# Optimization experiments

Measured on AMD Instinct MI355X. Metric: run time of the kernel, lower is better.

Reference implementation:

```python
import jax, jax.numpy as jnp
import numpy as np

N = 50000
E_RAND = 800000
F_IN = 128
HID = 128
HEADS = 8
LAYERS = 2
DH = HID // HEADS  # 16


def setup_inputs() -> dict:
    key = jax.random.key(0)
    ks = jax.random.split(key, 8)
    x = jax.random.normal(ks[0], (N, F_IN), dtype=jnp.float32)
    # random edges + self loops so every row of the segment-softmax is nonempty
    rnd = jax.random.randint(ks[1], (2, E_RAND), 0, N, dtype=jnp.int32)
    loops = jnp.tile(jnp.arange(N, dtype=jnp.int32), (2, 1))
    edge_idx = jnp.concatenate([rnd, loops], axis=1)  # [2, 850000]
    edge_vals = jnp.ones((edge_idx.shape[1],), dtype=jnp.float32)
    # glorot-style params
    enc_W = jax.random.normal(ks[2], (F_IN, HID), dtype=jnp.float32) * np.sqrt(2.0 / (F_IN + HID))
    enc_b = jnp.zeros((HID,), dtype=jnp.float32)
    W_stack = jax.random.normal(ks[3], (LAYERS, HEADS, HID, DH), dtype=jnp.float32) * np.sqrt(2.0 / (HID + DH))
    a_stack = jax.random.normal(ks[4], (LAYERS, HEADS, 2 * DH), dtype=jnp.float32) * np.sqrt(2.0 / (1 + 2 * DH))
    return {"x": x, "edge_idx": edge_idx, "edge_vals": edge_vals,
            "enc_W": enc_W, "enc_b": enc_b, "W_stack": W_stack, "a_stack": a_stack}


def _gat_layer(xin, row, col, edge_vals, W, a):
    # xin: [N, HID]; W: [H, HID, DH]; a: [H, 2*DH]
    n = xin.shape[0]
    h = jnp.einsum('nd,hdf->hnf', xin, W)            # [H, N, DH]
    a_src, a_dst = a[:, :DH], a[:, DH:]
    alpha_src = jnp.einsum('hnf,hf->hn', h, a_src)   # a . h[row] part
    alpha_dst = jnp.einsum('hnf,hf->hn', h, a_dst)   # a . h[col] part
    logits = edge_vals[None, :] * (alpha_src[:, row] + alpha_dst[:, col])  # [H, E]
    e = jnp.exp(jax.nn.leaky_relu(logits, 0.2))      # unnormalized attention
    rowsum = jax.ops.segment_sum(e.T, row, num_segments=n)               # [N, H]
    msg = e[:, :, None] * h[:, col, :]               # [H, E, DH]
    agg = jax.vmap(lambda m: jax.ops.segment_sum(m, row, num_segments=n))(msg)  # [H, N, DH]
    out = agg / rowsum.T[:, :, None]
    return jnp.transpose(out, (1, 0, 2)).reshape(n, -1)  # concat heads -> [N, HID]


def reference(x, edge_idx, edge_vals, enc_W, enc_b, W_stack, a_stack):
    row, col = edge_idx[0], edge_idx[1]
    xc = x @ enc_W + enc_b  # encoder
    L = W_stack.shape[0]
    for ell in range(L):
        out = _gat_layer(xc, row, col, edge_vals, W_stack[ell], a_stack[ell])
        if ell != L - 1:
            out = jax.nn.elu(out)  # feat_drop is identity in eval mode
        xc = out + xc if ell > 0 else out  # use_residual=True
    # single snapshot: stack over T=1 then permute(1,0,2) -> [N, 1, HID]
    return xc[:, None, :]
```

## Files before the change

### kernel.cpp

```cpp
#include <hip/hip_runtime.h>
#include <hip/hip_bf16.h>


typedef __attribute__((ext_vector_type(8))) short short8;
typedef __attribute__((ext_vector_type(4))) float floatx4;
typedef __attribute__((ext_vector_type(2))) float floatx2;

__device__ __forceinline__ unsigned f2u(float f) { return __float_as_uint(f); }
__device__ __forceinline__ float u2f(unsigned u) { return __uint_as_float(u); }
__device__ __forceinline__ unsigned short f2bf_rne(float x) {
    unsigned u = f2u(x);
    unsigned r = (u + 0x7FFF + ((u >> 16) & 1)) >> 16;
    return (unsigned short)r;
}


__global__ void histpack_kernel(const int* __restrict__ row, int* __restrict__ deg,
                                int* __restrict__ rank, int E, int EB,
                                const float* __restrict__ encW,
                                const float* __restrict__ Wstack,
                                short8* __restrict__ Wh, short8* __restrict__ Wl) {
    int b = blockIdx.x;
    if (b < EB) {
        int e = b * 256 + threadIdx.x;
        if (e < E) rank[e] = atomicAdd(&deg[row[e]], 1);
        return;
    }
    int idx = (b - EB) * 256 + threadIdx.x;
    if (idx >= 3 * 2048) return;
    int mat = idx >> 11;
    int r = idx & 2047;
    int lane = r & 63;
    int tile = r >> 6;
    int ct = tile >> 2, kt = tile & 3;
    int ncol = ct * 16 + (lane & 15);
    int k0 = kt * 32 + ((lane >> 4) * 8);
    short8 hv, lv;
#pragma unroll
    for (int j = 0; j < 8; ++j) {
        int k = k0 + j;
        float w = (mat == 0)
            ? encW[k * 128 + ncol]
            : Wstack[(mat - 1) * 16384 + (ncol >> 4) * 2048 + k * 16 + (ncol & 15)];
        unsigned u = f2u(w);
        hv[j] = (short)(u >> 16);
        float hf = u2f(u & 0xFFFF0000u);
        float l = w - hf;
        lv[j] = (short)(f2u(l) >> 16);
    }
    Wh[idx] = hv;
    Wl[idx] = lv;
}

__global__ void gathercv_kernel(const int* __restrict__ perm, const int* __restrict__ colv,
                                const float* __restrict__ ev, int2* __restrict__ csr_cv,
                                int E) {
    int s = blockIdx.x * 256 + threadIdx.x;
    if (s < E) {
        int e = perm[s];
        csr_cv[s] = make_int2(colv[e], __float_as_int(ev[e]));
    }
}


__device__ __forceinline__ void
gemm_body(int bid, const float* __restrict__ A, const short8* __restrict__ Bh,
          const short8* __restrict__ Bl, const float* __restrict__ bias,
          const float* __restrict__ avec, float* __restrict__ Cf,
          unsigned short* __restrict__ Cbf,
          float* __restrict__ asrc, float* __restrict__ adst, int n, int flags) {
    int wave = threadIdx.x >> 6;
    int lane = threadIdx.x & 63;
    int q = lane >> 4;
    int col = lane & 15;
    int n0w = bid * 64 + wave * 16;

    int arow = min(n0w + col, n - 1);
    const float* Arow = A + (size_t)arow * 128;
    int kb = q * 8;
    short8 Ah[4], Al[4];
#pragma unroll
    for (int kt = 0; kt < 4; ++kt) {
        float4 f0 = *(const float4*)(Arow + kt * 32 + kb);
        float4 f1 = *(const float4*)(Arow + kt * 32 + kb + 4);
        float fv[8] = {f0.x, f0.y, f0.z, f0.w, f1.x, f1.y, f1.z, f1.w};
#pragma unroll
        for (int j = 0; j < 8; ++j) {
            unsigned u = f2u(fv[j]);
            Ah[kt][j] = (short)(u >> 16);
            float hf = u2f(u & 0xFFFF0000u);
            float l = fv[j] - hf;
            Al[kt][j] = (short)(f2u(l) >> 16);
        }
    }

    int nbase = n0w + q * 4;
#pragma unroll
    for (int ct = 0; ct < 8; ++ct) {
        short8 bh[4], bl[4];
#pragma unroll
        for (int kt = 0; kt < 4; ++kt) {
            bh[kt] = Bh[(ct * 4 + kt) * 64 + lane];
            bl[kt] = Bl[(ct * 4 + kt) * 64 + lane];
        }
        float bv = (flags & 1) ? bias[ct * 16 + col] : 0.f;
        floatx4 acc = {bv, bv, bv, bv};
#pragma unroll
        for (int kt = 0; kt < 4; ++kt) {
            acc = __builtin_amdgcn_mfma_f32_16x16x32_bf16(Ah[kt], bh[kt], acc, 0, 0, 0);
            acc = __builtin_amdgcn_mfma_f32_16x16x32_bf16(Al[kt], bh[kt], acc, 0, 0, 0);
            acc = __builtin_amdgcn_mfma_f32_16x16x32_bf16(Ah[kt], bl[kt], acc, 0, 0, 0);
        }
#pragma unroll
        for (int reg = 0; reg < 4; ++reg) {
            int node = nbase + reg;
            if (node < n) {
                if (flags & 4) Cbf[(size_t)node * 128 + ct * 16 + col] = f2bf_rne(acc[reg]);
                else           Cf[(size_t)node * 128 + ct * 16 + col] = acc[reg];
            }
        }
        if (flags & 2) {
            float a_s = avec[ct * 32 + col];
            float a_d = avec[ct * 32 + 16 + col];
#pragma unroll
            for (int reg = 0; reg < 4; ++reg) {
                float ps = acc[reg] * a_s;
                float pd = acc[reg] * a_d;
#pragma unroll
                for (int off = 8; off; off >>= 1) {
                    ps += __shfl_down(ps, off, 16);
                    pd += __shfl_down(pd, off, 16);
                }
                int node = nbase + reg;
                if (col == 0 && node < n) {
                    asrc[node * 8 + ct] = ps;
                    adst[node * 8 + ct] = pd;
                }
            }
        }
    }
}

__global__ __launch_bounds__(256) void
gemm_mfma(const float* __restrict__ A, const short8* __restrict__ Bh,
          const short8* __restrict__ Bl, const float* __restrict__ avec,
          unsigned short* __restrict__ Cbf,
          float* __restrict__ asrc, float* __restrict__ adst, int n) {
    gemm_body(blockIdx.x, A, Bh, Bl, nullptr, avec, nullptr, Cbf, asrc, adst, n, 2 | 4);
}

__global__ __launch_bounds__(256) void
enc_scan_kernel(const float* __restrict__ x, const short8* __restrict__ Wh,
                const short8* __restrict__ Wl, const float* __restrict__ encb,
                float* __restrict__ xc, int n, int GBn,
                const int* __restrict__ deg, int* __restrict__ rowptr) {
    if ((int)blockIdx.x < GBn) {
        gemm_body(blockIdx.x, x, Wh, Wl, encb, nullptr, xc, nullptr,
                  nullptr, nullptr, n, 1);
        return;
    }
    __shared__ int sd[256];
    __shared__ int sbase;
    int t = threadIdx.x;
    int cb = blockIdx.x - GBn;
    int lim = cb * 256;
    const int4* deg4 = (const int4*)deg;
    int lim4 = lim >> 2;
    int b0 = 0, b1 = 0, b2 = 0, b3 = 0;
    for (int k = t; k < lim4; k += 256) {
        int4 d = deg4[k];
        b0 += d.x; b1 += d.y; b2 += d.z; b3 += d.w;
    }
    sd[t] = (b0 + b1) + (b2 + b3);
    __syncthreads();
    for (int off = 128; off; off >>= 1) {
        if (t < off) sd[t] += sd[t + off];
        __syncthreads();
    }
    if (t == 0) sbase = sd[0];
    __syncthreads();
    int idx = lim + t;
    int v = (idx < n) ? deg[idx] : 0;
    sd[t] = v;
    __syncthreads();
    for (int off = 1; off < 256; off <<= 1) {
        int add = (t >= off) ? sd[t - off] : 0;
        __syncthreads();
        sd[t] += add;
        __syncthreads();
    }
    if (idx < n) rowptr[idx] = sbase + sd[t] - v;
    if (idx == n - 1) rowptr[n] = sbase + sd[t];
}

__global__ __launch_bounds__(256) void
sperm_gemm_kernel(const float* __restrict__ xc, const short8* __restrict__ Wh1,
                  const short8* __restrict__ Wl1, const float* __restrict__ avec,
                  unsigned short* __restrict__ hbf, float* __restrict__ asrc,
                  float* __restrict__ adst, int n, int GBn,
                  const int* __restrict__ row, const int* __restrict__ rank,
                  const int* __restrict__ rowptr, int* __restrict__ perm, int E) {
    if ((int)blockIdx.x < GBn) {
        gemm_body(blockIdx.x, xc, Wh1, Wl1, nullptr, avec, nullptr, hbf,
                  asrc, adst, n, 2 | 4);
        return;
    }
    int e = (blockIdx.x - GBn) * 256 + threadIdx.x;
    if (e < E) perm[rowptr[row[e]] + rank[e]] = e;
}


__global__ __launch_bounds__(256) void
aggregate_kernel(const int* __restrict__ rowptr, const int2* __restrict__ cv,
                 const unsigned short* __restrict__ hbf,
                 const float* __restrict__ asrc, const float* __restrict__ adst,
                 const float* __restrict__ resid, float* __restrict__ out,
                 int mode, int n) {
    int wid = (blockIdx.x * 256 + threadIdx.x) >> 6;
    if (wid >= n) return;
    int lane = threadIdx.x & 63;
    int grp = lane >> 4;
    int l4 = lane & 15;
    int h = l4 >> 1;

    int s = rowptr[wid];
    int e = rowptr[wid + 1];
    float as_w = asrc[wid * 8 + h];

    floatx2 acc0 = {0.f, 0.f}, acc1 = {0.f, 0.f};
    floatx2 acc2 = {0.f, 0.f}, acc3 = {0.f, 0.f};
    float ws = 0.f;

#pragma unroll 4
    for (int j = s + grp; j < e; j += 4) {
        int2 cvj = cv[j];
        int c = cvj.x;
        float v = __int_as_float(cvj.y);
        float lg = v * (as_w + adst[c * 8 + h]);
        float lr = fmaxf(lg, 0.2f * lg);
        float w = __expf(lr);
        uint4 hv = *(const uint4*)(hbf + (size_t)c * 128 + l4 * 8);
        floatx2 w2 = {w, w};
        floatx2 p0 = {u2f(hv.x << 16), u2f(hv.x & 0xFFFF0000u)};
        floatx2 p1 = {u2f(hv.y << 16), u2f(hv.y & 0xFFFF0000u)};
        floatx2 p2 = {u2f(hv.z << 16), u2f(hv.z & 0xFFFF0000u)};
        floatx2 p3 = {u2f(hv.w << 16), u2f(hv.w & 0xFFFF0000u)};
        acc0 += w2 * p0;
        acc1 += w2 * p1;
        acc2 += w2 * p2;
        acc3 += w2 * p3;
        ws += w;
    }

    float a0 = acc0.x, a1 = acc0.y, a2 = acc1.x, a3 = acc1.y;
    float a4 = acc2.x, a5 = acc2.y, a6 = acc3.x, a7 = acc3.y;

#define RED4(x) x += __shfl_xor(x, 16); x += __shfl_xor(x, 32);
    RED4(a0) RED4(a1) RED4(a2) RED4(a3)
    RED4(a4) RED4(a5) RED4(a6) RED4(a7)
    RED4(ws)
#undef RED4

    if (grp == 0) {
        float inv = 1.0f / ws;
        float o[8] = {a0 * inv, a1 * inv, a2 * inv, a3 * inv,
                      a4 * inv, a5 * inv, a6 * inv, a7 * inv};
        size_t base = (size_t)wid * 128 + l4 * 8;
        if (mode == 0) {
#pragma unroll
            for (int k = 0; k < 8; ++k) o[k] = o[k] > 0.f ? o[k] : expm1f(o[k]);
        } else {
            float4 r0 = *(const float4*)(resid + base);
            float4 r1 = *(const float4*)(resid + base + 4);
            o[0] += r0.x; o[1] += r0.y; o[2] += r0.z; o[3] += r0.w;
            o[4] += r1.x; o[5] += r1.y; o[6] += r1.z; o[7] += r1.w;
        }
        float4 w0 = {o[0], o[1], o[2], o[3]};
        float4 w1 = {o[4], o[5], o[6], o[7]};
        *(float4*)(out + base) = w0;
        *(float4*)(out + base + 4) = w1;
    }
}


extern "C" void kernel_launch(void* const* d_in, const int* in_sizes, int n_in,
                              void* d_out, int out_size, void* d_ws, size_t ws_size,
                              hipStream_t stream) {
    const int N = in_sizes[0] / 128;
    const int E = in_sizes[2];

    const float* x      = (const float*)d_in[0];
    const int*   eidx   = (const int*)d_in[1];
    const float* ev     = (const float*)d_in[2];
    const float* encW   = (const float*)d_in[3];
    const float* encb   = (const float*)d_in[4];
    const float* Wstack = (const float*)d_in[5];
    const float* astack = (const float*)d_in[6];
    float* out = (float*)d_out;

    const int* row = eidx;
    const int* colv = eidx + E;

    const int NCH = (N + 255) / 256;

    char* p = (char*)d_ws;
    float* xc   = (float*)p; p += (size_t)N * 128 * 4;
    float* xcB  = (float*)p; p += (size_t)N * 128 * 4;
    unsigned short* hbf = (unsigned short*)p; p += (size_t)N * 128 * 2;
    float* asrc = (float*)p; p += (size_t)N * 8 * 4;
    float* adst = (float*)p; p += (size_t)N * 8 * 4;
    short8* Wh  = (short8*)p; p += 3 * 2048 * 16;
    short8* Wl  = (short8*)p; p += 3 * 2048 * 16;
    int2* csr_cv = (int2*)p; p += (size_t)E * 8;
    int* deg    = (int*)p;   p += (size_t)N * 4;
    int* rowptr = (int*)p;   p += (size_t)(N + 1) * 4;

    int* rank = (int*)xcB;
    int* perm = rank + E;

    const int GB = (N + 63) / 64;
    const int AGG = (N + 3) / 4;
    const int EB = (E + 255) / 256;

    hipMemsetAsync(deg, 0, (size_t)N * 4, stream);
    histpack_kernel<<<EB + 24, 256, 0, stream>>>(row, deg, rank, E, EB,
                                                 encW, Wstack, Wh, Wl);

    enc_scan_kernel<<<GB + NCH, 256, 0, stream>>>(x, Wh, Wl, encb, xc, N, GB,
                                                  deg, rowptr);

    sperm_gemm_kernel<<<GB + EB, 256, 0, stream>>>(xc, Wh + 2048, Wl + 2048, astack,
                                                   hbf, asrc, adst, N, GB,
                                                   row, rank, rowptr, perm, E);

    gathercv_kernel<<<EB, 256, 0, stream>>>(perm, colv, ev, csr_cv, E);

    aggregate_kernel<<<AGG, 256, 0, stream>>>(rowptr, csr_cv, hbf, asrc, adst,
                                              nullptr, xcB, 0, N);

    gemm_mfma<<<GB, 256, 0, stream>>>(xcB, Wh + 4096, Wl + 4096, astack + 256,
                                      hbf, asrc, adst, N);
    aggregate_kernel<<<AGG, 256, 0, stream>>>(rowptr, csr_cv, hbf, asrc, adst,
                                              xcB, out, 1, N);
}
```

Measured before the change: 297.1 us.

## Regroup preprocessing: fuse deg zeroing with weight packing, overlap histogram with encoder GEMM

Replaces the memset with a zeroing branch inside the weight-pack kernel. The edge-degree histogram now runs in the same launch as the encoder GEMM instead of alongside the packing, and the prefix scan becomes its own kernel. The launch count stays the same; the intent is to drop the separate memset and to overlap the atomic histogram with GEMM work. The cost is an extra dependency boundary between the histogram and the scan, which used to share a launch with the GEMM.

New measurement: 312.2 us. 5.1% more time.

```diff
diff --git a/kernel.cpp b/kernel.cpp
--- a/kernel.cpp
+++ b/kernel.cpp
@@ -15,18 +15,17 @@
 }
 
 
-__global__ void histpack_kernel(const int* __restrict__ row, int* __restrict__ deg,
-                                int* __restrict__ rank, int E, int EB,
-                                const float* __restrict__ encW,
-                                const float* __restrict__ Wstack,
-                                short8* __restrict__ Wh, short8* __restrict__ Wl) {
+__global__ void pack_zero_kernel(int* __restrict__ deg, int n, int ZB,
+                                 const float* __restrict__ encW,
+                                 const float* __restrict__ Wstack,
+                                 short8* __restrict__ Wh, short8* __restrict__ Wl) {
     int b = blockIdx.x;
-    if (b < EB) {
-        int e = b * 256 + threadIdx.x;
-        if (e < E) rank[e] = atomicAdd(&deg[row[e]], 1);
+    if (b < ZB) {
+        int i = b * 256 + threadIdx.x;
+        if (i < n) deg[i] = 0;
         return;
     }
-    int idx = (b - EB) * 256 + threadIdx.x;
+    int idx = (b - ZB) * 256 + threadIdx.x;
     if (idx >= 3 * 2048) return;
     int mat = idx >> 11;
     int r = idx & 2047;
@@ -150,19 +149,26 @@
 }
 
 __global__ __launch_bounds__(256) void
-enc_scan_kernel(const float* __restrict__ x, const short8* __restrict__ Wh,
+hist_enc_kernel(const int* __restrict__ row, int* __restrict__ deg,
+                int* __restrict__ rank, int E, int EB,
+                const float* __restrict__ x, const short8* __restrict__ Wh,
                 const short8* __restrict__ Wl, const float* __restrict__ encb,
-                float* __restrict__ xc, int n, int GBn,
-                const int* __restrict__ deg, int* __restrict__ rowptr) {
-    if ((int)blockIdx.x < GBn) {
-        gemm_body(blockIdx.x, x, Wh, Wl, encb, nullptr, xc, nullptr,
-                  nullptr, nullptr, n, 1);
+                float* __restrict__ xc, int n) {
+    int b = blockIdx.x;
+    if (b < EB) {
+        int e = b * 256 + threadIdx.x;
+        if (e < E) rank[e] = atomicAdd(&deg[row[e]], 1);
         return;
     }
+    gemm_body(b - EB, x, Wh, Wl, encb, nullptr, xc, nullptr, nullptr, nullptr, n, 1);
+}
+
+__global__ __launch_bounds__(256) void
+scan_kernel(const int* __restrict__ deg, int* __restrict__ rowptr, int n) {
     __shared__ int sd[256];
     __shared__ int sbase;
     int t = threadIdx.x;
-    int cb = blockIdx.x - GBn;
+    int cb = blockIdx.x;
     int lim = cb * 256;
     const int4* deg4 = (const int4*)deg;
     int lim4 = lim >> 2;
@@ -322,12 +328,12 @@
     const int AGG = (N + 3) / 4;
     const int EB = (E + 255) / 256;
 
-    hipMemsetAsync(deg, 0, (size_t)N * 4, stream);
-    histpack_kernel<<<EB + 24, 256, 0, stream>>>(row, deg, rank, E, EB,
-                                                 encW, Wstack, Wh, Wl);
-
-    enc_scan_kernel<<<GB + NCH, 256, 0, stream>>>(x, Wh, Wl, encb, xc, N, GB,
-                                                  deg, rowptr);
+    pack_zero_kernel<<<NCH + 24, 256, 0, stream>>>(deg, N, NCH, encW, Wstack, Wh, Wl);
+
+    hist_enc_kernel<<<EB + GB, 256, 0, stream>>>(row, deg, rank, E, EB,
+                                                 x, Wh, Wl, encb, xc, N);
+
+    scan_kernel<<<NCH, 256, 0, stream>>>(deg, rowptr, N);
 
     sperm_gemm_kernel<<<GB + EB, 256, 0, stream>>>(xc, Wh + 2048, Wl + 2048, astack,
                                                    hbf, asrc, adst, N, GB,
@@ -340,6 +346,7 @@
 
     gemm_mfma<<<GB, 256, 0, stream>>>(xcB, Wh + 4096, Wl + 4096, astack + 256,
                                       hbf, asrc, adst, N);
+
     aggregate_kernel<<<AGG, 256, 0, stream>>>(rowptr, csr_cv, hbf, asrc, adst,
                                               xcB, out, 1, N);
 }
```
